# Optimization experiments

Measured on AMD Instinct MI355X. Metric: run time of the kernel, lower is better.

The kernel has to match this reference:

```python
import jax, jax.numpy as jnp
import numpy as np

DIM = 2048
HEADS = 16
HEAD_DIM = 128
KV_HEADS = 8
ROPE_BASE = 10000.0


def _rope_tables(seq_len):
    inv_freq = 1.0 / (ROPE_BASE ** (jnp.arange(0, HEAD_DIM, 2, dtype=jnp.float32) / HEAD_DIM))
    t = jnp.arange(seq_len, dtype=jnp.float32)
    freqs = jnp.outer(t, inv_freq)              # [S, D/2]
    emb = jnp.concatenate([freqs, freqs], -1)    # [S, D]
    return jnp.cos(emb), jnp.sin(emb)


def _rotate_half(x):
    x1, x2 = jnp.split(x, 2, axis=-1)
    return jnp.concatenate([-x2, x1], axis=-1)


def setup_inputs() -> dict:
    key = jax.random.key(0)
    ks = jax.random.split(key, 5)
    B, S = 2, 2048
    s = 0.02
    return {
        "x": jax.random.normal(ks[0], (B, S, DIM), jnp.float32),
        "Wq": jax.random.normal(ks[1], (DIM, HEADS * HEAD_DIM), jnp.float32) * s,
        "Wk": jax.random.normal(ks[2], (DIM, KV_HEADS * HEAD_DIM), jnp.float32) * s,
        "Wv": jax.random.normal(ks[3], (DIM, KV_HEADS * HEAD_DIM), jnp.float32) * s,
        "Wo": jax.random.normal(ks[4], (HEADS * HEAD_DIM, DIM), jnp.float32) * s,
    }


def reference(x, Wq, Wk, Wv, Wo):
    B, S, _ = x.shape
    scale = 1.0 / np.sqrt(HEAD_DIM).astype(np.float32)
    q = (x @ Wq).reshape(B, S, HEADS, HEAD_DIM)
    k = (x @ Wk).reshape(B, S, KV_HEADS, HEAD_DIM)
    v = (x @ Wv).reshape(B, S, KV_HEADS, HEAD_DIM)
    cos, sin = _rope_tables(S)                   # [S, D]
    cos = cos[None, :, None, :]                  # broadcast over batch, heads
    sin = sin[None, :, None, :]
    q = q * cos + _rotate_half(q) * sin
    k = k * cos + _rotate_half(k) * sin
    q = jnp.transpose(q, (0, 2, 1, 3))           # [B,H,S,D]
    k = jnp.transpose(k, (0, 2, 1, 3))           # [B,Hkv,S,D]
    v = jnp.transpose(v, (0, 2, 1, 3))
    rep = HEADS // KV_HEADS
    k = jnp.repeat(k, rep, axis=1)               # GQA -> [B,H,S,D]
    v = jnp.repeat(v, rep, axis=1)
    scores = jnp.einsum('bhid,bhjd->bhij', q, k) * scale
    causal = jnp.tril(jnp.ones((S, S), dtype=bool))
    scores = jnp.where(causal, scores, -jnp.inf)
    attn = jax.nn.softmax(scores, axis=-1)
    out = jnp.einsum('bhij,bhjd->bhid', attn, v)
    out = jnp.transpose(out, (0, 2, 1, 3)).reshape(B, S, HEADS * HEAD_DIM)
    return out @ Wo
```

## Files before the change

### kernel.cpp

```cpp
#include <hip/hip_runtime.h>

#define DIMX 2048
#define SEQ  2048
#define BATCH 2
#define NH   16
#define NKV  8
#define HD   128
#define MTOK (BATCH*SEQ)
#define NQKV 4096
#define QKLD 3072

typedef __bf16 bf16x8 __attribute__((ext_vector_type(8)));
typedef float  f32x4  __attribute__((ext_vector_type(4)));
typedef float  f32x16 __attribute__((ext_vector_type(16)));
typedef unsigned short u16x8 __attribute__((ext_vector_type(8)));
typedef unsigned short u16x4 __attribute__((ext_vector_type(4)));
typedef unsigned int   u32x4 __attribute__((ext_vector_type(4)));

__device__ __forceinline__ unsigned short f2bf(float f) {
    unsigned u = __builtin_bit_cast(unsigned, f);
    u += 0x7fffu + ((u >> 16) & 1u);
    return (unsigned short)(u >> 16);
}
__device__ __forceinline__ float bf2f(unsigned short h) {
    unsigned u = ((unsigned)h) << 16;
    return __builtin_bit_cast(float, u);
}

__device__ __forceinline__ void gload16(const void* g, void* l) {
    __builtin_amdgcn_global_load_lds(
        (const __attribute__((address_space(1))) unsigned int*)g,
        (__attribute__((address_space(3))) unsigned int*)l, 16, 0, 0);
}

__global__ __launch_bounds__(256) void k_convert(const float* __restrict__ in,
                                                 unsigned short* __restrict__ out, int n8) {
    int i = blockIdx.x * 256 + threadIdx.x;
    if (i >= n8) return;
    f32x4 a = ((const f32x4*)in)[(size_t)i*2];
    f32x4 b = ((const f32x4*)in)[(size_t)i*2+1];
    u16x8 o;
    o[0]=f2bf(a[0]); o[1]=f2bf(a[1]); o[2]=f2bf(a[2]); o[3]=f2bf(a[3]);
    o[4]=f2bf(b[0]); o[5]=f2bf(b[1]); o[6]=f2bf(b[2]); o[7]=f2bf(b[3]);
    ((u16x8*)out)[i] = o;
}

__global__ __launch_bounds__(256) void k_transpose(const float* __restrict__ W,
                                                   unsigned short* __restrict__ Wt,
                                                   int K, int N) {
    __shared__ unsigned short tile[64*65];
    int t = threadIdx.x;
    int n0 = blockIdx.x * 64, k0 = blockIdx.y * 64;
    #pragma unroll
    for (int i = 0; i < 16; ++i) {
        int idx = t + i*256, r = idx >> 6, c = idx & 63;
        tile[r*65+c] = f2bf(W[(size_t)(k0+r)*N + n0 + c]);
    }
    __syncthreads();
    #pragma unroll
    for (int i = 0; i < 16; ++i) {
        int idx = t + i*256, n = idx >> 6, k = idx & 63;
        Wt[(size_t)(n0+n)*K + k0 + k] = tile[k*65+n];
    }
}

template<int NREP, int MODE>
__global__ __launch_bounds__(512, 2) void k_gemm256(const unsigned short* __restrict__ A,
                                                    const unsigned short* __restrict__ Bt,
                                                    void* __restrict__ Cv,
                                                    unsigned short* __restrict__ Vt,
                                                    int M, int N, int K, int ldc) {
    constexpr int BN  = NREP * 64;
    constexpr int BWC = NREP * 16;
    __shared__ __align__(16) char As[2][32768];
    __shared__ __align__(16) char Bs[2][BN * 128];
    int bid = blockIdx.x;
    int rem = (bid & 7) * 32 + (bid >> 3);
    int bx = rem & 15, by = rem >> 4;
    int row0 = by * 256, col0 = bx * BN;
    int tid = threadIdx.x, wave = tid >> 6, lane = tid & 63;
    int wr = wave >> 2, wc = wave & 3;
    int g = lane >> 4, r16 = lane & 15;
    const char* Ab = (const char*)A;
    const char* Bb = (const char*)Bt;

    f32x4 acc[8][NREP] = {};

    auto STAGE = [&](int buf, int t) {
        int k0b = t * 128;
        #pragma unroll
        for (int p = 0; p < 4; ++p) {
            int c = wave * 4 + p;
            int o = c * 1024 + lane * 16;
            int row = o >> 7;
            int colb = (o & 127) ^ ((row & 7) << 4);
            gload16(Ab + (size_t)(row0 + row) * (size_t)(K * 2) + k0b + colb, &As[buf][c * 1024]);
        }
        #pragma unroll
        for (int p = 0; p < NREP; ++p) {
            int c = wave * NREP + p;
            int o = c * 1024 + lane * 16;
            int row = o >> 7;
            int colb = (o & 127) ^ ((row & 7) << 4);
            gload16(Bb + (size_t)(col0 + row) * (size_t)(K * 2) + k0b + colb, &Bs[buf][c * 1024]);
        }
    };

    int nt = K >> 6;
    STAGE(0, 0);
    STAGE(1, 1);
    if constexpr (NREP == 4) asm volatile("s_waitcnt vmcnt(8)" ::: "memory");
    else                     asm volatile("s_waitcnt vmcnt(6)" ::: "memory");
    __builtin_amdgcn_s_barrier();

    for (int t = 0; t < nt; ++t) {
        int buf = t & 1;
        const char* AL = As[buf];
        const char* BL = Bs[buf];
        bf16x8 a0[4][2], a1[4][2], bfr[NREP][2];
        #pragma unroll
        for (int mi = 0; mi < 4; ++mi)
            #pragma unroll
            for (int s = 0; s < 2; ++s) {
                int r = wr*128 + mi*16 + r16;
                int o = r*128 + s*64 + g*16;
                a0[mi][s] = *(const bf16x8*)(AL + (o ^ ((r & 7) << 4)));
            }
        #pragma unroll
        for (int ni = 0; ni < NREP; ++ni)
            #pragma unroll
            for (int s = 0; s < 2; ++s) {
                int r = wc*BWC + ni*16 + r16;
                int o = r*128 + s*64 + g*16;
                bfr[ni][s] = *(const bf16x8*)(BL + (o ^ ((r & 7) << 4)));
            }
        __builtin_amdgcn_s_setprio(1);
        #pragma unroll
        for (int mi = 0; mi < 4; ++mi)
            #pragma unroll
            for (int ni = 0; ni < NREP; ++ni)
                #pragma unroll
                for (int s = 0; s < 2; ++s)
                    acc[mi][ni] = __builtin_amdgcn_mfma_f32_16x16x32_bf16(a0[mi][s], bfr[ni][s], acc[mi][ni], 0, 0, 0);
        __builtin_amdgcn_s_setprio(0);
        #pragma unroll
        for (int mi = 0; mi < 4; ++mi)
            #pragma unroll
            for (int s = 0; s < 2; ++s) {
                int r = wr*128 + 64 + mi*16 + r16;
                int o = r*128 + s*64 + g*16;
                a1[mi][s] = *(const bf16x8*)(AL + (o ^ ((r & 7) << 4)));
            }
        asm volatile("s_waitcnt lgkmcnt(0)" ::: "memory");
        __builtin_amdgcn_sched_barrier(0);
        __builtin_amdgcn_s_barrier();
        if (t + 2 < nt) STAGE(buf, t + 2);
        __builtin_amdgcn_sched_barrier(0);
        __builtin_amdgcn_s_setprio(1);
        #pragma unroll
        for (int mi = 0; mi < 4; ++mi)
            #pragma unroll
            for (int ni = 0; ni < NREP; ++ni)
                #pragma unroll
                for (int s = 0; s < 2; ++s)
                    acc[mi+4][ni] = __builtin_amdgcn_mfma_f32_16x16x32_bf16(a1[mi][s], bfr[ni][s], acc[mi+4][ni], 0, 0, 0);
        __builtin_amdgcn_s_setprio(0);
        if (t + 2 < nt) {
            if constexpr (NREP == 4) asm volatile("s_waitcnt vmcnt(8)" ::: "memory");
            else                     asm volatile("s_waitcnt vmcnt(6)" ::: "memory");
        } else {
            asm volatile("s_waitcnt vmcnt(0)" ::: "memory");
        }
        __builtin_amdgcn_s_barrier();
    }

    #pragma unroll
    for (int mi = 0; mi < 8; ++mi)
        #pragma unroll
        for (int ni = 0; ni < NREP; ++ni) {
            if (MODE == 0 && col0 >= 3072) {
                int vcol = col0 + wc*BWC + ni*16 + r16 - 3072;
                int d = vcol & 127, kh = vcol >> 7;
                int row = row0 + wr*128 + mi*16 + g*4;
                int b = row >> 11, s = row & (SEQ-1);
                u16x4 pk;
                #pragma unroll
                for (int rr = 0; rr < 4; ++rr) pk[rr] = f2bf(acc[mi][ni][rr]);
                *(u16x4*)&Vt[((size_t)(b*NKV + kh)*HD + d)*SEQ + s] = pk;
            } else {
                #pragma unroll
                for (int rr = 0; rr < 4; ++rr) {
                    int row = row0 + wr*128 + mi*16 + g*4 + rr;
                    int col = col0 + wc*BWC + ni*16 + r16;
                    float v = acc[mi][ni][rr];
                    if (MODE == 1) ((float*)Cv)[(size_t)row*ldc + col] = v;
                    else ((unsigned short*)Cv)[(size_t)row*ldc + col] = f2bf(v);
                }
            }
        }
}

__global__ __launch_bounds__(256) void k_rope(unsigned short* __restrict__ qkv) {
    int tid = blockIdx.x * 256 + threadIdx.x;
    int i    = tid & 63;
    int rest = tid >> 6;
    int head = rest % (NH + NKV);
    int tok  = rest / (NH + NKV);
    int pos  = tok & (SEQ - 1);
    size_t base = (size_t)tok * QKLD + head*HD;
    float x1 = bf2f(qkv[base + i]);
    float x2 = bf2f(qkv[base + i + 64]);
    float inv = exp2f(-0.20762050593046014f * (float)i);
    float ang = (float)pos * inv;
    float s, c;
    sincosf(ang, &s, &c);
    float sc = (head < NH) ? 0.12754984523341717f : 1.0f;
    qkv[base + i]      = f2bf((x1*c - x2*s) * sc);
    qkv[base + i + 64] = f2bf((x2*c + x1*s) * sc);
}

__global__ __launch_bounds__(256) void k_attn(const unsigned short* __restrict__ qkv,
                                              const unsigned short* __restrict__ Vt,
                                              unsigned short* __restrict__ attn_out) {
    __shared__ __align__(16) char KVs[2][32768];
    int bid = blockIdx.x;
    int xcd = bid & 7, idx = bid >> 3;
    int bh  = xcd * 4 + (idx >> 3);
    int p   = idx & 7;
    int b = bh >> 4, h = bh & 15, kvh = h >> 1;
    int tid = threadIdx.x, wave = tid >> 6, lane = tid & 63;
    int l31 = lane & 31, hi = lane >> 5;
    int nt0 = 2*p + 2;
    constexpr int NT = 34;
    int q0w = p*128 + wave*32;
    int qg  = q0w + l31;
    const unsigned short* qbase = qkv + (size_t)(b*SEQ)*QKLD;
    const char* kbase = (const char*)(qbase + DIMX + kvh*HD);
    const char* vbase = (const char*)(Vt + ((size_t)(b*NKV + kvh)*HD)*SEQ);

    bf16x8 qf[8];
    auto loadQ = [&](int qrow) {
        const unsigned short* qr = qbase + (size_t)qrow*QKLD + h*HD;
        #pragma unroll
        for (int s2 = 0; s2 < 8; ++s2) qf[s2] = *(const bf16x8*)(qr + s2*16 + hi*8);
    };
    loadQ(qg);

    f32x16 acc[4] = {};
    float mrow = -1e30f, lrow = 0.f;

    auto STAGE = [&](int v, int buf) {
        int kv0 = (v < nt0 ? v : v - nt0) * 64;
        char* KL = KVs[buf];
        char* VL = KL + 16384;
        #pragma unroll
        for (int pp = 0; pp < 4; ++pp) {
            int c = wave*4 + pp;
            int row  = c*4 + (lane >> 4);
            int colb = ((lane & 15) * 16) ^ ((row & 7) << 4);
            gload16(kbase + (size_t)(kv0 + row)*(QKLD*2) + colb, KL + c*1024);
            int d    = c*8 + (lane >> 3);
            int colv = ((lane & 7) * 16) ^ ((d & 7) << 4);
            gload16(vbase + (size_t)d*(SEQ*2) + (size_t)kv0*2 + colv, VL + c*1024);
        }
    };

    auto writeOut = [&]() {
        float inv = 1.0f / lrow;
        #pragma unroll
        for (int dt = 0; dt < 4; ++dt)
            #pragma unroll
            for (int qd = 0; qd < 4; ++qd) {
                u16x4 o4;
                #pragma unroll
                for (int j = 0; j < 4; ++j) o4[j] = f2bf(acc[dt][qd*4 + j] * inv);
                *(u16x4*)&attn_out[(size_t)(b*SEQ + qg)*DIMX + h*HD + dt*32 + qd*8 + hi*4] = o4;
            }
    };

    STAGE(0, 0);
    asm volatile("s_waitcnt vmcnt(0)" ::: "memory");
    __syncthreads();

    for (int v = 0; v < NT; ++v) {
        int buf = v & 1;
        int kv0 = (v < nt0 ? v : v - nt0) * 64;
        if (v + 1 < NT) STAGE(v + 1, buf ^ 1);
        const char* KL = KVs[buf];
        const char* VL = KL + 16384;
        if (kv0 <= q0w + 31) {
            f32x16 st0 = {}, st1 = {};
            const char* kr0 = KL + l31*256;
            const char* kr1 = KL + (32 + l31)*256;
            unsigned sw = (unsigned)((l31 & 7) << 4);
            __builtin_amdgcn_s_setprio(1);
            #pragma unroll
            for (int s2 = 0; s2 < 8; ++s2) {
                unsigned off = (unsigned)(s2*32 + hi*16);
                bf16x8 kf0 = *(const bf16x8*)(kr0 + (off ^ sw));
                bf16x8 kf1 = *(const bf16x8*)(kr1 + (off ^ sw));
                st0 = __builtin_amdgcn_mfma_f32_32x32x16_bf16(kf0, qf[s2], st0, 0, 0, 0);
                st1 = __builtin_amdgcn_mfma_f32_32x32x16_bf16(kf1, qf[s2], st1, 0, 0, 0);
            }
            __builtin_amdgcn_s_setprio(0);
            if (kv0 + 63 > q0w) {
                #pragma unroll
                for (int r = 0; r < 16; ++r) {
                    int kvr = kv0 + (r & 3) + 8*(r >> 2) + 4*hi;
                    st0[r] = (kvr      <= qg) ? st0[r] : -1e30f;
                    st1[r] = (kvr + 32 <= qg) ? st1[r] : -1e30f;
                }
            }
            float mt = -1e30f;
            #pragma unroll
            for (int r = 0; r < 16; ++r) { mt = fmaxf(mt, st0[r]); mt = fmaxf(mt, st1[r]); }
            mt = fmaxf(mt, __shfl_xor(mt, 32, 64));
            if (!__all(mt - mrow <= 8.0f)) {
                float mn = fmaxf(mrow, mt);
                float corr = exp2f(mrow - mn);
                mrow = mn; lrow *= corr;
                #pragma unroll
                for (int dt = 0; dt < 4; ++dt)
                    #pragma unroll
                    for (int r = 0; r < 16; ++r) acc[dt][r] *= corr;
            }
            float rs = 0.f;
            #pragma unroll
            for (int r = 0; r < 16; ++r) {
                float p0 = exp2f(st0[r] - mrow); st0[r] = p0; rs += p0;
                float p1 = exp2f(st1[r] - mrow); st1[r] = p1; rs += p1;
            }
            lrow += rs + __shfl_xor(rs, 32, 64);
            #pragma unroll
            for (int t = 0; t < 2; ++t)
                #pragma unroll
                for (int ks = 0; ks < 2; ++ks) {
                    const f32x16& stt = t ? st1 : st0;
                    int rb = ks * 8;
                    float p0 = stt[rb+0], p1 = stt[rb+1], p2 = stt[rb+2], p3 = stt[rb+3];
                    float p4 = stt[rb+4], p5 = stt[rb+5], p6 = stt[rb+6], p7 = stt[rb+7];
                    unsigned w0, w1, w2, w3;
                    asm("v_cvt_pk_bf16_f32 %0, %1, %2" : "=v"(w0) : "v"(p0), "v"(p1));
                    asm("v_cvt_pk_bf16_f32 %0, %1, %2" : "=v"(w1) : "v"(p2), "v"(p3));
                    asm("v_cvt_pk_bf16_f32 %0, %1, %2" : "=v"(w2) : "v"(p4), "v"(p5));
                    asm("v_cvt_pk_bf16_f32 %0, %1, %2" : "=v"(w3) : "v"(p6), "v"(p7));
                    asm("v_permlane32_swap_b32 %0, %1" : "+v"(w0), "+v"(w2));
                    asm("v_permlane32_swap_b32 %0, %1" : "+v"(w1), "+v"(w3));
                    u32x4 pu = {w0, w1, w2, w3};
                    bf16x8 pfrag = __builtin_bit_cast(bf16x8, pu);
                    int ks4 = t*2 + ks;
                    __builtin_amdgcn_s_setprio(1);
                    #pragma unroll
                    for (int dt = 0; dt < 4; ++dt) {
                        int d = dt*32 + l31;
                        bf16x8 vf = *(const bf16x8*)(VL + d*128 +
                                     (((unsigned)(ks4*32 + hi*16)) ^ ((unsigned)((d & 7) << 4))));
                        acc[dt] = __builtin_amdgcn_mfma_f32_32x32x16_bf16(vf, pfrag, acc[dt], 0, 0, 0);
                    }
                    __builtin_amdgcn_s_setprio(0);
                }
        }
        asm volatile("s_waitcnt vmcnt(0)" ::: "memory");
        __syncthreads();
        if (v == nt0 - 1) {
            writeOut();
            #pragma unroll
            for (int dt = 0; dt < 4; ++dt)
                #pragma unroll
                for (int r = 0; r < 16; ++r) acc[dt][r] = 0.f;
            mrow = -1e30f; lrow = 0.f;
            q0w = (15 - p)*128 + wave*32;
            qg  = q0w + l31;
            loadQ(qg);
        }
    }
    writeOut();
}

extern "C" void kernel_launch(void* const* d_in, const int* in_sizes, int n_in,
                              void* d_out, int out_size, void* d_ws, size_t ws_size,
                              hipStream_t stream) {
    const float* x  = (const float*)d_in[0];
    const float* Wq = (const float*)d_in[1];
    const float* Wk = (const float*)d_in[2];
    const float* Wv = (const float*)d_in[3];
    const float* Wo = (const float*)d_in[4];

    unsigned short* xb   = (unsigned short*)d_ws;
    unsigned short* Wtq  = xb  + (size_t)MTOK*DIMX;
    unsigned short* Wto  = Wtq + (size_t)NQKV*DIMX;
    unsigned short* qkv  = Wto + (size_t)DIMX*DIMX;
    unsigned short* aout = qkv + (size_t)MTOK*QKLD;
    unsigned short* Vt   = aout + (size_t)MTOK*DIMX;

    k_convert<<<(MTOK*DIMX/8 + 255)/256, 256, 0, stream>>>(x, xb, MTOK*DIMX/8);

    dim3 tg32(DIMX/64, DIMX/64);
    dim3 tg16(1024/64, DIMX/64);
    k_transpose<<<tg32, 256, 0, stream>>>(Wq, Wtq,                         DIMX, DIMX);
    k_transpose<<<tg16, 256, 0, stream>>>(Wk, Wtq + (size_t)2048*DIMX,     DIMX, 1024);
    k_transpose<<<tg16, 256, 0, stream>>>(Wv, Wtq + (size_t)3072*DIMX,     DIMX, 1024);
    k_transpose<<<tg32, 256, 0, stream>>>(Wo, Wto,                         DIMX, DIMX);

    k_gemm256<4, 0><<<256, 512, 0, stream>>>(xb, Wtq, qkv, Vt, MTOK, NQKV, DIMX, QKLD);

    k_rope<<<(MTOK*(NH+NKV)*64)/256, 256, 0, stream>>>(qkv);

    k_attn<<<256, 256, 0, stream>>>(qkv, Vt, aout);

    k_gemm256<2, 1><<<256, 512, 0, stream>>>(aout, Wto, (float*)d_out, nullptr, MTOK, DIMX, DIMX, DIMX);
}
```

Before: 234.8 us.

## Split paired causal query tiles into separate attention blocks, two blocks per CU

Each attention block previously processed two query tiles (p and 15-p) back to back for causal load balance. The change launches 512 blocks, one query tile each, and sets launch bounds to two blocks per CU, so the two tiles run concurrently on a CU instead of sequentially. This aims to raise occupancy and latency hiding. In exchange, per-block work is uneven and the scheduler must balance it, and register pressure is capped by the occupancy bound.

```diff
diff --git a/kernel.cpp b/kernel.cpp
--- a/kernel.cpp
+++ b/kernel.cpp
@@ -219,38 +219,39 @@
     qkv[base + i + 64] = f2bf((x2*c + x1*s) * sc);
 }
 
-__global__ __launch_bounds__(256) void k_attn(const unsigned short* __restrict__ qkv,
-                                              const unsigned short* __restrict__ Vt,
-                                              unsigned short* __restrict__ attn_out) {
+__global__ __launch_bounds__(256, 2) void k_attn(const unsigned short* __restrict__ qkv,
+                                                 const unsigned short* __restrict__ Vt,
+                                                 unsigned short* __restrict__ attn_out) {
     __shared__ __align__(16) char KVs[2][32768];
     int bid = blockIdx.x;
-    int xcd = bid & 7, idx = bid >> 3;
+    int half = bid >> 8;
+    int rem  = bid & 255;
+    int xcd = rem & 7, idx = rem >> 3;
     int bh  = xcd * 4 + (idx >> 3);
     int p   = idx & 7;
+    int qt  = half ? (15 - p) : p;
     int b = bh >> 4, h = bh & 15, kvh = h >> 1;
     int tid = threadIdx.x, wave = tid >> 6, lane = tid & 63;
     int l31 = lane & 31, hi = lane >> 5;
-    int nt0 = 2*p + 2;
-    constexpr int NT = 34;
-    int q0w = p*128 + wave*32;
+    int nt = 2*qt + 2;
+    int q0w = qt*128 + wave*32;
     int qg  = q0w + l31;
     const unsigned short* qbase = qkv + (size_t)(b*SEQ)*QKLD;
     const char* kbase = (const char*)(qbase + DIMX + kvh*HD);
     const char* vbase = (const char*)(Vt + ((size_t)(b*NKV + kvh)*HD)*SEQ);
 
     bf16x8 qf[8];
-    auto loadQ = [&](int qrow) {
-        const unsigned short* qr = qbase + (size_t)qrow*QKLD + h*HD;
+    {
+        const unsigned short* qr = qbase + (size_t)qg*QKLD + h*HD;
         #pragma unroll
         for (int s2 = 0; s2 < 8; ++s2) qf[s2] = *(const bf16x8*)(qr + s2*16 + hi*8);
-    };
-    loadQ(qg);
+    }
 
     f32x16 acc[4] = {};
     float mrow = -1e30f, lrow = 0.f;
 
     auto STAGE = [&](int v, int buf) {
-        int kv0 = (v < nt0 ? v : v - nt0) * 64;
+        int kv0 = v * 64;
         char* KL = KVs[buf];
         char* VL = KL + 16384;
         #pragma unroll
@@ -265,27 +266,14 @@
         }
     };
 
-    auto writeOut = [&]() {
-        float inv = 1.0f / lrow;
-        #pragma unroll
-        for (int dt = 0; dt < 4; ++dt)
-            #pragma unroll
-            for (int qd = 0; qd < 4; ++qd) {
-                u16x4 o4;
-                #pragma unroll
-                for (int j = 0; j < 4; ++j) o4[j] = f2bf(acc[dt][qd*4 + j] * inv);
-                *(u16x4*)&attn_out[(size_t)(b*SEQ + qg)*DIMX + h*HD + dt*32 + qd*8 + hi*4] = o4;
-            }
-    };
-
     STAGE(0, 0);
     asm volatile("s_waitcnt vmcnt(0)" ::: "memory");
     __syncthreads();
 
-    for (int v = 0; v < NT; ++v) {
+    for (int v = 0; v < nt; ++v) {
         int buf = v & 1;
-        int kv0 = (v < nt0 ? v : v - nt0) * 64;
-        if (v + 1 < NT) STAGE(v + 1, buf ^ 1);
+        int kv0 = v * 64;
+        if (v + 1 < nt) STAGE(v + 1, buf ^ 1);
         const char* KL = KVs[buf];
         const char* VL = KL + 16384;
         if (kv0 <= q0w + 31) {
@@ -362,19 +350,18 @@
         }
         asm volatile("s_waitcnt vmcnt(0)" ::: "memory");
         __syncthreads();
-        if (v == nt0 - 1) {
-            writeOut();
-            #pragma unroll
-            for (int dt = 0; dt < 4; ++dt)
-                #pragma unroll
-                for (int r = 0; r < 16; ++r) acc[dt][r] = 0.f;
-            mrow = -1e30f; lrow = 0.f;
-            q0w = (15 - p)*128 + wave*32;
-            qg  = q0w + l31;
-            loadQ(qg);
-        }
-    }
-    writeOut();
+    }
+
+    float inv = 1.0f / lrow;
+    #pragma unroll
+    for (int dt = 0; dt < 4; ++dt)
+        #pragma unroll
+        for (int qd = 0; qd < 4; ++qd) {
+            u16x4 o4;
+            #pragma unroll
+            for (int j = 0; j < 4; ++j) o4[j] = f2bf(acc[dt][qd*4 + j] * inv);
+            *(u16x4*)&attn_out[(size_t)(b*SEQ + qg)*DIMX + h*HD + dt*32 + qd*8 + hi*4] = o4;
+        }
 }
 
 extern "C" void kernel_launch(void* const* d_in, const int* in_sizes, int n_in,
@@ -406,7 +393,7 @@
 
     k_rope<<<(MTOK*(NH+NKV)*64)/256, 256, 0, stream>>>(qkv);
 
-    k_attn<<<256, 256, 0, stream>>>(qkv, Vt, aout);
+    k_attn<<<512, 256, 0, stream>>>(qkv, Vt, aout);
 
     k_gemm256<2, 1><<<256, 512, 0, stream>>>(aout, Wto, (float*)d_out, nullptr, MTOK, DIMX, DIMX, DIMX);
 }
```

After: 215.8 us, median of 2. 1.09x faster.
